# Kernel optimization log

Measured on AMD Instinct MI355X. Metric: run time of the kernel, lower is better.

The kernel has to match this reference:

```python
import jax, jax.numpy as jnp
import numpy as np

N = 65536   # total sentences
B = 8192    # number of bags (ragged scopes)
C = 1024    # class_dim
R = 100     # rel_num


def setup_inputs() -> dict:
    key = jax.random.key(0)
    k1, k2, k3, k4 = jax.random.split(key, 4)
    X = jax.random.normal(k1, (N, C), jnp.float32)            # post-fc1 sentence reps
    Constraints = jax.random.normal(k2, (R, C), jnp.float32)  # post-fc2 constraint reps
    W = jax.random.normal(k3, (R, C), jnp.float32) * 0.02     # classifier weight
    b = jnp.zeros((R,), jnp.float32)                           # classifier bias
    # ragged scopes: random cut points -> contiguous [start, end) per bag
    rng = np.random.default_rng(0)
    cuts = np.sort(rng.choice(np.arange(1, N), B - 1, replace=False))
    starts = np.concatenate([[0], cuts])
    ends = np.concatenate([cuts, [N]])
    X_Scope = jnp.asarray(np.stack([starts, ends], axis=1), jnp.int32)  # [B, 2]
    X_Rel = jax.random.randint(k4, (B,), 0, R, jnp.int32)               # [B]
    return dict(X=X, Constraints=Constraints, W=W, b=b, X_Scope=X_Scope, X_Rel=X_Rel)


def reference(X, Constraints, W, b, X_Scope, X_Rel):
    n, _ = X.shape
    nb = X_Scope.shape[0]
    # map each sentence to its (contiguous) bag via scope starts
    starts = X_Scope[:, 0]
    seg = jnp.searchsorted(starts, jnp.arange(n, dtype=starts.dtype), side='right') - 1  # [N]
    # per-sentence attention logit against its bag's relation constraint
    Con = Constraints[X_Rel]                                   # [B, C]
    scores = jnp.einsum('nc,nc->n', X, Con[seg])               # [N]
    # numerically-stable per-bag softmax
    m = jax.ops.segment_max(scores, seg, num_segments=nb)      # [B]
    e = jnp.exp(scores - m[seg])                               # [N]
    denom = jax.ops.segment_sum(e, seg, num_segments=nb)       # [B]
    w = e / denom[seg]                                         # [N]
    # attention-weighted bag pooling
    bag = jax.ops.segment_sum(w[:, None] * X, seg, num_segments=nb)  # [B, C]
    # classifier (dropout is identity at eval)
    return bag @ W.T + b                                       # [B, R]
```

## Files before the change

kernel.cpp:

```cpp
#include <hip/hip_runtime.h>
#include <math.h>

#define CDIM 1024
#define RDIM 100
#define NBAGS 8192
#define RPAD 112

typedef float floatx4 __attribute__((ext_vector_type(4)));
typedef short bf16x8 __attribute__((ext_vector_type(8)));

__device__ __forceinline__ float dot4(float4 a, float4 b) {
    return a.x * b.x + a.y * b.y + a.z * b.z + a.w * b.w;
}

__device__ __forceinline__ unsigned short f2bf(float f) {
    unsigned int u = __builtin_bit_cast(unsigned int, f);
    u += 0x7FFFu + ((u >> 16) & 1u);
    return (unsigned short)(u >> 16);
}

#define LOADROW(D0, D1, D2, D3, ri)                                          \
    {                                                                        \
        const float4* p_ = (const float4*)(X + (size_t)(ri) * CDIM);         \
        D0 = p_[lane];       D1 = p_[lane + 64];                             \
        D2 = p_[lane + 128]; D3 = p_[lane + 192];                            \
    }

#define COMPUTE_ROW(A0, A1, A2, A3)                                          \
    {                                                                        \
        float p = dot4(A0, c0) + dot4(A1, c1) + dot4(A2, c2) + dot4(A3, c3); \
        p += __shfl_xor(p, 1);                                               \
        p += __shfl_xor(p, 2);                                               \
        p += __shfl_xor(p, 4);                                               \
        p += __shfl_xor(p, 8);                                               \
        p += __shfl_xor(p, 16);                                              \
        p += __shfl_xor(p, 32);                                              \
        const float newm = fmaxf(m, p);                                      \
        const float corr = __expf(m - newm);             \
        const float wgt  = __expf(p - newm);                                 \
        denom = fmaf(denom, corr, wgt);                                      \
        a0.x = fmaf(a0.x, corr, wgt * A0.x); a0.y = fmaf(a0.y, corr, wgt * A0.y); \
        a0.z = fmaf(a0.z, corr, wgt * A0.z); a0.w = fmaf(a0.w, corr, wgt * A0.w); \
        a1.x = fmaf(a1.x, corr, wgt * A1.x); a1.y = fmaf(a1.y, corr, wgt * A1.y); \
        a1.z = fmaf(a1.z, corr, wgt * A1.z); a1.w = fmaf(a1.w, corr, wgt * A1.w); \
        a2.x = fmaf(a2.x, corr, wgt * A2.x); a2.y = fmaf(a2.y, corr, wgt * A2.y); \
        a2.z = fmaf(a2.z, corr, wgt * A2.z); a2.w = fmaf(a2.w, corr, wgt * A2.w); \
        a3.x = fmaf(a3.x, corr, wgt * A3.x); a3.y = fmaf(a3.y, corr, wgt * A3.y); \
        a3.z = fmaf(a3.z, corr, wgt * A3.z); a3.w = fmaf(a3.w, corr, wgt * A3.w); \
        m = newm;                                                            \
    }

__global__ __launch_bounds__(256) void bag_softmax_kernel(
    const float* __restrict__ X,
    const float* __restrict__ Constraints,
    const int* __restrict__ scope,
    const int* __restrict__ rel,
    const float* __restrict__ W,
    unsigned short* __restrict__ bagbuf,
    unsigned short* __restrict__ PW)
{
    const int lane = threadIdx.x & 63;
    const int w    = threadIdx.x >> 6;

    if (blockIdx.x >= NBAGS) {
        const int rr = blockIdx.x - NBAGS;
        const int t  = threadIdx.x;
        const int kc  = t >> 3;
        const int sub = (t >> 1) & 3;
        const int i0  = (t & 1) * 4;
        ushort4 o = {0, 0, 0, 0};
        if (rr < RDIM) {
            float4 v = *(const float4*)(W + (size_t)rr * CDIM + t * 4);
            o.x = f2bf(v.x); o.y = f2bf(v.y); o.z = f2bf(v.z); o.w = f2bf(v.w);
        }
        const int tt = rr >> 4, rl = rr & 15;
        *(ushort4*)(PW + ((size_t)(kc * 7 + tt) * 64 + sub * 16 + rl) * 8 + i0) = o;
        return;
    }

    __shared__ float4 lds_acc[4][256];
    __shared__ float  lds_m[4];
    __shared__ float  lds_d[4];

    const int bag = blockIdx.x;
    const int s = scope[2 * bag];
    const int e = scope[2 * bag + 1];
    const int r = rel[bag];

    const float4* conp = (const float4*)(Constraints + (size_t)r * CDIM);
    const float4 c0 = conp[lane];
    const float4 c1 = conp[lane + 64];
    const float4 c2 = conp[lane + 128];
    const float4 c3 = conp[lane + 192];

    float4 a0 = {0.f, 0.f, 0.f, 0.f};
    float4 a1 = {0.f, 0.f, 0.f, 0.f};
    float4 a2 = {0.f, 0.f, 0.f, 0.f};
    float4 a3 = {0.f, 0.f, 0.f, 0.f};
    float m = -INFINITY;
    float denom = 0.f;

    int row = s + w;
    if (row < e) {
        float4 A0, A1, A2, A3;
        float4 B0, B1, B2, B3;
        float4 C0, C1, C2, C3;

        LOADROW(A0, A1, A2, A3, row)
        if (row + 4 < e) LOADROW(B0, B1, B2, B3, row + 4)

        for (; row + 8 < e; row += 4) {
            LOADROW(C0, C1, C2, C3, row + 8)
            __builtin_amdgcn_sched_barrier(0);
            COMPUTE_ROW(A0, A1, A2, A3)
            A0 = B0; A1 = B1; A2 = B2; A3 = B3;
            B0 = C0; B1 = C1; B2 = C2; B3 = C3;
        }
        if (row + 4 < e) {
            COMPUTE_ROW(A0, A1, A2, A3)
            COMPUTE_ROW(B0, B1, B2, B3)
        } else {
            COMPUTE_ROW(A0, A1, A2, A3)
        }
    }

    if (lane == 0) { lds_m[w] = m; lds_d[w] = denom; }
    lds_acc[w][lane]       = a0;
    lds_acc[w][lane + 64]  = a1;
    lds_acc[w][lane + 128] = a2;
    lds_acc[w][lane + 192] = a3;
    __syncthreads();

    const int t = threadIdx.x;
    const float m0 = lds_m[0], m1 = lds_m[1], m2 = lds_m[2], m3 = lds_m[3];
    const float ms = fmaxf(fmaxf(m0, m1), fmaxf(m2, m3));
    const float f0 = __expf(m0 - ms);
    const float f1 = __expf(m1 - ms);
    const float f2 = __expf(m2 - ms);
    const float f3 = __expf(m3 - ms);
    const float dn = f0 * lds_d[0] + f1 * lds_d[1] + f2 * lds_d[2] + f3 * lds_d[3];
    const float inv = 1.0f / dn;

    const float4 v0 = lds_acc[0][t];
    const float4 v1 = lds_acc[1][t];
    const float4 v2 = lds_acc[2][t];
    const float4 v3 = lds_acc[3][t];
    const float ox = (f0 * v0.x + f1 * v1.x + f2 * v2.x + f3 * v3.x) * inv;
    const float oy = (f0 * v0.y + f1 * v1.y + f2 * v2.y + f3 * v3.y) * inv;
    const float oz = (f0 * v0.z + f1 * v1.z + f2 * v2.z + f3 * v3.z) * inv;
    const float ow = (f0 * v0.w + f1 * v1.w + f2 * v2.w + f3 * v3.w) * inv;

    ushort4 o;
    o.x = f2bf(ox); o.y = f2bf(oy); o.z = f2bf(oz); o.w = f2bf(ow);
    *(ushort4*)(bagbuf + (size_t)bag * CDIM + t * 4) = o;
}

__global__ __launch_bounds__(512) void bag_gemm_mfma(
    const unsigned short* __restrict__ bagbuf,
    const unsigned short* __restrict__ PW,
    const float* __restrict__ bias,
    float* __restrict__ out)
{
    const int q    = threadIdx.x >> 6;
    const int lane = threadIdx.x & 63;
    const int bag0 = blockIdx.x * 16;
    const int ln15 = lane & 15;
    const int koff = (lane >> 4) * 8;

    __shared__ floatx4 lds[8][7][64];

    floatx4 acc[7];
    #pragma unroll
    for (int t = 0; t < 7; ++t) acc[t] = (floatx4){0.f, 0.f, 0.f, 0.f};

    const unsigned short* aRow  = bagbuf + (size_t)(bag0 + ln15) * CDIM + koff;
    const unsigned short* bBase = PW + lane * 8;

    #pragma unroll
    for (int i = 0; i < 4; ++i) {
        const int kc = q * 4 + i;
        const bf16x8 a = *(const bf16x8*)(aRow + kc * 32);
        #pragma unroll
        for (int t = 0; t < 7; ++t) {
            const bf16x8 b = *(const bf16x8*)(bBase + (size_t)(kc * 7 + t) * 512);
            acc[t] = __builtin_amdgcn_mfma_f32_16x16x32_bf16(a, b, acc[t], 0, 0, 0);
        }
    }

    #pragma unroll
    for (int t = 0; t < 7; ++t) lds[q][t][lane] = acc[t];
    __syncthreads();

    const int p = threadIdx.x;
    if (p < 448) {
        const int t    = p >> 6;
        const int slot = p & 63;
        const int r    = t * 16 + (slot & 15);
        if (r < RDIM) {
            floatx4 s = lds[0][t][slot];
            #pragma unroll
            for (int qq = 1; qq < 8; ++qq) s += lds[qq][t][slot];
            const float bv = bias[r];
            const int bagr = bag0 + (slot >> 4) * 4;
            out[(size_t)(bagr + 0) * RDIM + r] = s[0] + bv;
            out[(size_t)(bagr + 1) * RDIM + r] = s[1] + bv;
            out[(size_t)(bagr + 2) * RDIM + r] = s[2] + bv;
            out[(size_t)(bagr + 3) * RDIM + r] = s[3] + bv;
        }
    }
}

extern "C" void kernel_launch(void* const* d_in, const int* in_sizes, int n_in,
                              void* d_out, int out_size, void* d_ws, size_t ws_size,
                              hipStream_t stream) {
    const float* X    = (const float*)d_in[0];
    const float* Con  = (const float*)d_in[1];
    const float* W    = (const float*)d_in[2];
    const float* bias = (const float*)d_in[3];
    const int* scope  = (const int*)d_in[4];
    const int* rel    = (const int*)d_in[5];
    float* out = (float*)d_out;

    unsigned short* bagbuf = (unsigned short*)d_ws;
    unsigned short* PW     = bagbuf + (size_t)NBAGS * CDIM;

    bag_softmax_kernel<<<NBAGS + RPAD, 256, 0, stream>>>(X, Con, scope, rel, W, bagbuf, PW);
    bag_gemm_mfma<<<NBAGS / 16, 512, 0, stream>>>(bagbuf, PW, bias, out);
}
```

Baseline: 63.86 us.

## Fuse bag softmax pooling with classifier GEMM via shared-memory bag tile

Each block now processes 16 bags in sequence. Their pooled bf16 vectors go into a swizzled shared-memory tile instead of a global workspace, and the MFMA classifier for those 16 bags runs inside the same kernel. The W conversion to packed bf16 moves to a small separate prep kernel, and the next bag's constraint row is prefetched during the current bag. This removes the global round trip for the bag buffer and the second large kernel launch. In exchange the grid drops from about 8K blocks to 512, which limits memory-level parallelism for the bandwidth-bound scan over X and serialises bags with block barriers.

```diff
diff --git a/kernel.cpp b/kernel.cpp
--- a/kernel.cpp
+++ b/kernel.cpp
@@ -5,6 +5,8 @@
 #define RDIM 100
 #define NBAGS 8192
 #define RPAD 112
+#define BPB 16
+#define NBLK (NBAGS / BPB)
 
 typedef float floatx4 __attribute__((ext_vector_type(4)));
 typedef short bf16x8 __attribute__((ext_vector_type(8)));
@@ -50,162 +52,161 @@
         m = newm;                                                            \
     }
 
-__global__ __launch_bounds__(256) void bag_softmax_kernel(
+__global__ __launch_bounds__(256) void pw_prep(
+    const float* __restrict__ W, unsigned short* __restrict__ PW)
+{
+    const int rr = blockIdx.x;
+    const int t  = threadIdx.x;
+    const int kc  = t >> 3;
+    const int sub = (t >> 1) & 3;
+    const int i0  = (t & 1) * 4;
+    ushort4 o = {0, 0, 0, 0};
+    if (rr < RDIM) {
+        float4 v = *(const float4*)(W + (size_t)rr * CDIM + t * 4);
+        o.x = f2bf(v.x); o.y = f2bf(v.y); o.z = f2bf(v.z); o.w = f2bf(v.w);
+    }
+    const int tt = rr >> 4, rl = rr & 15;
+    *(ushort4*)(PW + ((size_t)(kc * 7 + tt) * 64 + sub * 16 + rl) * 8 + i0) = o;
+}
+
+__global__ __launch_bounds__(256) void fused_kernel(
     const float* __restrict__ X,
     const float* __restrict__ Constraints,
     const int* __restrict__ scope,
     const int* __restrict__ rel,
-    const float* __restrict__ W,
-    unsigned short* __restrict__ bagbuf,
-    unsigned short* __restrict__ PW)
-{
-    const int lane = threadIdx.x & 63;
-    const int w    = threadIdx.x >> 6;
-
-    if (blockIdx.x >= NBAGS) {
-        const int rr = blockIdx.x - NBAGS;
-        const int t  = threadIdx.x;
-        const int kc  = t >> 3;
-        const int sub = (t >> 1) & 3;
-        const int i0  = (t & 1) * 4;
-        ushort4 o = {0, 0, 0, 0};
-        if (rr < RDIM) {
-            float4 v = *(const float4*)(W + (size_t)rr * CDIM + t * 4);
-            o.x = f2bf(v.x); o.y = f2bf(v.y); o.z = f2bf(v.z); o.w = f2bf(v.w);
-        }
-        const int tt = rr >> 4, rl = rr & 15;
-        *(ushort4*)(PW + ((size_t)(kc * 7 + tt) * 64 + sub * 16 + rl) * 8 + i0) = o;
-        return;
-    }
-
-    __shared__ float4 lds_acc[4][256];
-    __shared__ float  lds_m[4];
-    __shared__ float  lds_d[4];
-
-    const int bag = blockIdx.x;
-    const int s = scope[2 * bag];
-    const int e = scope[2 * bag + 1];
-    const int r = rel[bag];
-
-    const float4* conp = (const float4*)(Constraints + (size_t)r * CDIM);
-    const float4 c0 = conp[lane];
-    const float4 c1 = conp[lane + 64];
-    const float4 c2 = conp[lane + 128];
-    const float4 c3 = conp[lane + 192];
-
-    float4 a0 = {0.f, 0.f, 0.f, 0.f};
-    float4 a1 = {0.f, 0.f, 0.f, 0.f};
-    float4 a2 = {0.f, 0.f, 0.f, 0.f};
-    float4 a3 = {0.f, 0.f, 0.f, 0.f};
-    float m = -INFINITY;
-    float denom = 0.f;
-
-    int row = s + w;
-    if (row < e) {
-        float4 A0, A1, A2, A3;
-        float4 B0, B1, B2, B3;
-        float4 C0, C1, C2, C3;
-
-        LOADROW(A0, A1, A2, A3, row)
-        if (row + 4 < e) LOADROW(B0, B1, B2, B3, row + 4)
-
-        for (; row + 8 < e; row += 4) {
-            LOADROW(C0, C1, C2, C3, row + 8)
-            __builtin_amdgcn_sched_barrier(0);
-            COMPUTE_ROW(A0, A1, A2, A3)
-            A0 = B0; A1 = B1; A2 = B2; A3 = B3;
-            B0 = C0; B1 = C1; B2 = C2; B3 = C3;
-        }
-        if (row + 4 < e) {
-            COMPUTE_ROW(A0, A1, A2, A3)
-            COMPUTE_ROW(B0, B1, B2, B3)
-        } else {
-            COMPUTE_ROW(A0, A1, A2, A3)
-        }
-    }
-
-    if (lane == 0) { lds_m[w] = m; lds_d[w] = denom; }
-    lds_acc[w][lane]       = a0;
-    lds_acc[w][lane + 64]  = a1;
-    lds_acc[w][lane + 128] = a2;
-    lds_acc[w][lane + 192] = a3;
-    __syncthreads();
-
-    const int t = threadIdx.x;
-    const float m0 = lds_m[0], m1 = lds_m[1], m2 = lds_m[2], m3 = lds_m[3];
-    const float ms = fmaxf(fmaxf(m0, m1), fmaxf(m2, m3));
-    const float f0 = __expf(m0 - ms);
-    const float f1 = __expf(m1 - ms);
-    const float f2 = __expf(m2 - ms);
-    const float f3 = __expf(m3 - ms);
-    const float dn = f0 * lds_d[0] + f1 * lds_d[1] + f2 * lds_d[2] + f3 * lds_d[3];
-    const float inv = 1.0f / dn;
-
-    const float4 v0 = lds_acc[0][t];
-    const float4 v1 = lds_acc[1][t];
-    const float4 v2 = lds_acc[2][t];
-    const float4 v3 = lds_acc[3][t];
-    const float ox = (f0 * v0.x + f1 * v1.x + f2 * v2.x + f3 * v3.x) * inv;
-    const float oy = (f0 * v0.y + f1 * v1.y + f2 * v2.y + f3 * v3.y) * inv;
-    const float oz = (f0 * v0.z + f1 * v1.z + f2 * v2.z + f3 * v3.z) * inv;
-    const float ow = (f0 * v0.w + f1 * v1.w + f2 * v2.w + f3 * v3.w) * inv;
-
-    ushort4 o;
-    o.x = f2bf(ox); o.y = f2bf(oy); o.z = f2bf(oz); o.w = f2bf(ow);
-    *(ushort4*)(bagbuf + (size_t)bag * CDIM + t * 4) = o;
-}
-
-__global__ __launch_bounds__(512) void bag_gemm_mfma(
-    const unsigned short* __restrict__ bagbuf,
     const unsigned short* __restrict__ PW,
     const float* __restrict__ bias,
     float* __restrict__ out)
 {
-    const int q    = threadIdx.x >> 6;
+    __shared__ float4 mergebuf[4][256];
+    __shared__ float  lds_m[4];
+    __shared__ float  lds_d[4];
+    __shared__ unsigned short bagsm[BPB][CDIM];
+
     const int lane = threadIdx.x & 63;
-    const int bag0 = blockIdx.x * 16;
+    const int w    = threadIdx.x >> 6;
+    const int t    = threadIdx.x;
+    const int bag0 = blockIdx.x * BPB;
+
+    float4 c0, c1, c2, c3;
+    {
+        const float4* conp = (const float4*)(Constraints + (size_t)rel[bag0] * CDIM);
+        c0 = conp[lane]; c1 = conp[lane + 64]; c2 = conp[lane + 128]; c3 = conp[lane + 192];
+    }
+
+    #pragma unroll 1
+    for (int j = 0; j < BPB; ++j) {
+        const int bag = bag0 + j;
+        const int s = scope[2 * bag];
+        const int e = scope[2 * bag + 1];
+
+        float4 a0 = {0.f, 0.f, 0.f, 0.f};
+        float4 a1 = {0.f, 0.f, 0.f, 0.f};
+        float4 a2 = {0.f, 0.f, 0.f, 0.f};
+        float4 a3 = {0.f, 0.f, 0.f, 0.f};
+        float m = -INFINITY;
+        float denom = 0.f;
+
+        int row = s + w;
+        if (row < e) {
+            float4 A0, A1, A2, A3;
+            float4 B0, B1, B2, B3;
+            float4 C0, C1, C2, C3;
+
+            LOADROW(A0, A1, A2, A3, row)
+            if (row + 4 < e) LOADROW(B0, B1, B2, B3, row + 4)
+
+            for (; row + 8 < e; row += 4) {
+                LOADROW(C0, C1, C2, C3, row + 8)
+                __builtin_amdgcn_sched_barrier(0);
+                COMPUTE_ROW(A0, A1, A2, A3)
+                A0 = B0; A1 = B1; A2 = B2; A3 = B3;
+                B0 = C0; B1 = C1; B2 = C2; B3 = C3;
+            }
+            if (row + 4 < e) {
+                COMPUTE_ROW(A0, A1, A2, A3)
+                COMPUTE_ROW(B0, B1, B2, B3)
+            } else {
+                COMPUTE_ROW(A0, A1, A2, A3)
+            }
+        }
+
+        float4 n0, n1, n2, n3;
+        if (j + 1 < BPB) {
+            const float4* conp = (const float4*)(Constraints + (size_t)rel[bag + 1] * CDIM);
+            n0 = conp[lane]; n1 = conp[lane + 64]; n2 = conp[lane + 128]; n3 = conp[lane + 192];
+        }
+
+        if (lane == 0) { lds_m[w] = m; lds_d[w] = denom; }
+        mergebuf[w][lane]       = a0;
+        mergebuf[w][lane + 64]  = a1;
+        mergebuf[w][lane + 128] = a2;
+        mergebuf[w][lane + 192] = a3;
+        __syncthreads();
+
+        const float m0 = lds_m[0], m1 = lds_m[1], m2 = lds_m[2], m3 = lds_m[3];
+        const float ms = fmaxf(fmaxf(m0, m1), fmaxf(m2, m3));
+        const float f0 = __expf(m0 - ms);
+        const float f1 = __expf(m1 - ms);
+        const float f2 = __expf(m2 - ms);
+        const float f3 = __expf(m3 - ms);
+        const float dn = f0 * lds_d[0] + f1 * lds_d[1] + f2 * lds_d[2] + f3 * lds_d[3];
+        const float inv = 1.0f / dn;
+
+        const float4 v0 = mergebuf[0][t];
+        const float4 v1 = mergebuf[1][t];
+        const float4 v2 = mergebuf[2][t];
+        const float4 v3 = mergebuf[3][t];
+        const float ox = (f0 * v0.x + f1 * v1.x + f2 * v2.x + f3 * v3.x) * inv;
+        const float oy = (f0 * v0.y + f1 * v1.y + f2 * v2.y + f3 * v3.y) * inv;
+        const float oz = (f0 * v0.z + f1 * v1.z + f2 * v2.z + f3 * v3.z) * inv;
+        const float ow = (f0 * v0.w + f1 * v1.w + f2 * v2.w + f3 * v3.w) * inv;
+
+        ushort4 o;
+        o.x = f2bf(ox); o.y = f2bf(oy); o.z = f2bf(oz); o.w = f2bf(ow);
+        const int blk = (t >> 1) ^ (j & 7);
+        *(ushort4*)((char*)&bagsm[j][0] + blk * 16 + (t & 1) * 8) = o;
+        __syncthreads();
+
+        c0 = n0; c1 = n1; c2 = n2; c3 = n3;
+    }
+
     const int ln15 = lane & 15;
-    const int koff = (lane >> 4) * 8;
-
-    __shared__ floatx4 lds[8][7][64];
-
-    floatx4 acc[7];
-    #pragma unroll
-    for (int t = 0; t < 7; ++t) acc[t] = (floatx4){0.f, 0.f, 0.f, 0.f};
-
-    const unsigned short* aRow  = bagbuf + (size_t)(bag0 + ln15) * CDIM + koff;
-    const unsigned short* bBase = PW + lane * 8;
-
-    #pragma unroll
-    for (int i = 0; i < 4; ++i) {
-        const int kc = q * 4 + i;
-        const bf16x8 a = *(const bf16x8*)(aRow + kc * 32);
-        #pragma unroll
-        for (int t = 0; t < 7; ++t) {
-            const bf16x8 b = *(const bf16x8*)(bBase + (size_t)(kc * 7 + t) * 512);
-            acc[t] = __builtin_amdgcn_mfma_f32_16x16x32_bf16(a, b, acc[t], 0, 0, 0);
-        }
-    }
-
-    #pragma unroll
-    for (int t = 0; t < 7; ++t) lds[q][t][lane] = acc[t];
-    __syncthreads();
-
-    const int p = threadIdx.x;
-    if (p < 448) {
-        const int t    = p >> 6;
-        const int slot = p & 63;
-        const int r    = t * 16 + (slot & 15);
+    const int kgrp = lane >> 4;
+    const int tA = w, tB = w + 4;
+    floatx4 accA = (floatx4){0.f, 0.f, 0.f, 0.f};
+    floatx4 accB = (floatx4){0.f, 0.f, 0.f, 0.f};
+    const bool hasB = (tB < 7);
+
+    #pragma unroll 4
+    for (int kc = 0; kc < CDIM / 32; ++kc) {
+        const int swz = (kc * 4 + kgrp) ^ (ln15 & 7);
+        const bf16x8 a = *(const bf16x8*)((const char*)&bagsm[ln15][0] + swz * 16);
+        const bf16x8 bA = *(const bf16x8*)(PW + ((size_t)(kc * 7 + tA) * 64 + lane) * 8);
+        accA = __builtin_amdgcn_mfma_f32_16x16x32_bf16(a, bA, accA, 0, 0, 0);
+        if (hasB) {
+            const bf16x8 bB = *(const bf16x8*)(PW + ((size_t)(kc * 7 + tB) * 64 + lane) * 8);
+            accB = __builtin_amdgcn_mfma_f32_16x16x32_bf16(a, bB, accB, 0, 0, 0);
+        }
+    }
+
+    const int mbase = kgrp * 4;
+    {
+        const int r = tA * 16 + ln15;
         if (r < RDIM) {
-            floatx4 s = lds[0][t][slot];
+            const float bv = bias[r];
             #pragma unroll
-            for (int qq = 1; qq < 8; ++qq) s += lds[qq][t][slot];
+            for (int reg = 0; reg < 4; ++reg)
+                out[(size_t)(bag0 + mbase + reg) * RDIM + r] = accA[reg] + bv;
+        }
+    }
+    if (hasB) {
+        const int r = tB * 16 + ln15;
+        if (r < RDIM) {
             const float bv = bias[r];
-            const int bagr = bag0 + (slot >> 4) * 4;
-            out[(size_t)(bagr + 0) * RDIM + r] = s[0] + bv;
-            out[(size_t)(bagr + 1) * RDIM + r] = s[1] + bv;
-            out[(size_t)(bagr + 2) * RDIM + r] = s[2] + bv;
-            out[(size_t)(bagr + 3) * RDIM + r] = s[3] + bv;
+            #pragma unroll
+            for (int reg = 0; reg < 4; ++reg)
+                out[(size_t)(bag0 + mbase + reg) * RDIM + r] = accB[reg] + bv;
         }
     }
 }
@@ -221,9 +222,8 @@
     const int* rel    = (const int*)d_in[5];
     float* out = (float*)d_out;
 
-    unsigned short* bagbuf = (unsigned short*)d_ws;
-    unsigned short* PW     = bagbuf + (size_t)NBAGS * CDIM;
-
-    bag_softmax_kernel<<<NBAGS + RPAD, 256, 0, stream>>>(X, Con, scope, rel, W, bagbuf, PW);
-    bag_gemm_mfma<<<NBAGS / 16, 512, 0, stream>>>(bagbuf, PW, bias, out);
-}
+    unsigned short* PW = (unsigned short*)d_ws;
+
+    pw_prep<<<RPAD, 256, 0, stream>>>(W, PW);
+    fused_kernel<<<NBLK, 256, 0, stream>>>(X, Con, scope, rel, PW, bias, out);
+}
```

Measured after the change: 68.29 us. +6.9%, slower.

## Defer per-bag wave merge from softmax kernel into GEMM kernel

Applied to the files above, without the earlier changes.

Each wave of the softmax kernel now writes its unnormalized bf16 partial accumulator and its running max/denominator to global memory, instead of merging across waves through LDS with a block barrier. The GEMM kernel computes the merge scales per bag and combines the four partials on the fly while building the MFMA A operand. This removes the shared-memory staging and barrier from the bandwidth-bound pass. In exchange it adds several times more intermediate global traffic, and partials are rounded to bf16 before merging.

```diff
diff --git a/kernel.cpp b/kernel.cpp
--- a/kernel.cpp
+++ b/kernel.cpp
@@ -17,6 +17,10 @@
     unsigned int u = __builtin_bit_cast(unsigned int, f);
     u += 0x7FFFu + ((u >> 16) & 1u);
     return (unsigned short)(u >> 16);
+}
+
+__device__ __forceinline__ float bf2f(unsigned short u) {
+    return __builtin_bit_cast(float, (unsigned int)u << 16);
 }
 
 #define LOADROW(D0, D1, D2, D3, ri)                                          \
@@ -50,13 +54,14 @@
         m = newm;                                                            \
     }
 
-__global__ __launch_bounds__(256) void bag_softmax_kernel(
+__global__ __launch_bounds__(256) void bag_softmax_partial(
     const float* __restrict__ X,
     const float* __restrict__ Constraints,
     const int* __restrict__ scope,
     const int* __restrict__ rel,
     const float* __restrict__ W,
-    unsigned short* __restrict__ bagbuf,
+    unsigned short* __restrict__ partial,
+    float* __restrict__ pmd,
     unsigned short* __restrict__ PW)
 {
     const int lane = threadIdx.x & 63;
@@ -78,10 +83,6 @@
         return;
     }
 
-    __shared__ float4 lds_acc[4][256];
-    __shared__ float  lds_m[4];
-    __shared__ float  lds_d[4];
-
     const int bag = blockIdx.x;
     const int s = scope[2 * bag];
     const int e = scope[2 * bag + 1];
@@ -124,39 +125,32 @@
         }
     }
 
-    if (lane == 0) { lds_m[w] = m; lds_d[w] = denom; }
-    lds_acc[w][lane]       = a0;
-    lds_acc[w][lane + 64]  = a1;
-    lds_acc[w][lane + 128] = a2;
-    lds_acc[w][lane + 192] = a3;
-    __syncthreads();
-
-    const int t = threadIdx.x;
-    const float m0 = lds_m[0], m1 = lds_m[1], m2 = lds_m[2], m3 = lds_m[3];
-    const float ms = fmaxf(fmaxf(m0, m1), fmaxf(m2, m3));
-    const float f0 = __expf(m0 - ms);
-    const float f1 = __expf(m1 - ms);
-    const float f2 = __expf(m2 - ms);
-    const float f3 = __expf(m3 - ms);
-    const float dn = f0 * lds_d[0] + f1 * lds_d[1] + f2 * lds_d[2] + f3 * lds_d[3];
-    const float inv = 1.0f / dn;
-
-    const float4 v0 = lds_acc[0][t];
-    const float4 v1 = lds_acc[1][t];
-    const float4 v2 = lds_acc[2][t];
-    const float4 v3 = lds_acc[3][t];
-    const float ox = (f0 * v0.x + f1 * v1.x + f2 * v2.x + f3 * v3.x) * inv;
-    const float oy = (f0 * v0.y + f1 * v1.y + f2 * v2.y + f3 * v3.y) * inv;
-    const float oz = (f0 * v0.z + f1 * v1.z + f2 * v2.z + f3 * v3.z) * inv;
-    const float ow = (f0 * v0.w + f1 * v1.w + f2 * v2.w + f3 * v3.w) * inv;
-
-    ushort4 o;
-    o.x = f2bf(ox); o.y = f2bf(oy); o.z = f2bf(oz); o.w = f2bf(ow);
-    *(ushort4*)(bagbuf + (size_t)bag * CDIM + t * 4) = o;
-}
-
-__global__ __launch_bounds__(512) void bag_gemm_mfma(
-    const unsigned short* __restrict__ bagbuf,
+    if (lane == 0) {
+        pmd[bag * 8 + w * 2 + 0] = m;
+        pmd[bag * 8 + w * 2 + 1] = denom;
+    }
+    unsigned short* pr = partial + ((size_t)bag * 4 + w) * CDIM;
+    {
+        ushort4 o; o.x = f2bf(a0.x); o.y = f2bf(a0.y); o.z = f2bf(a0.z); o.w = f2bf(a0.w);
+        *(ushort4*)(pr + 4 * lane) = o;
+    }
+    {
+        ushort4 o; o.x = f2bf(a1.x); o.y = f2bf(a1.y); o.z = f2bf(a1.z); o.w = f2bf(a1.w);
+        *(ushort4*)(pr + 256 + 4 * lane) = o;
+    }
+    {
+        ushort4 o; o.x = f2bf(a2.x); o.y = f2bf(a2.y); o.z = f2bf(a2.z); o.w = f2bf(a2.w);
+        *(ushort4*)(pr + 512 + 4 * lane) = o;
+    }
+    {
+        ushort4 o; o.x = f2bf(a3.x); o.y = f2bf(a3.y); o.z = f2bf(a3.z); o.w = f2bf(a3.w);
+        *(ushort4*)(pr + 768 + 4 * lane) = o;
+    }
+}
+
+__global__ __launch_bounds__(512) void bag_gemm_merge(
+    const unsigned short* __restrict__ partial,
+    const float* __restrict__ pmd,
     const unsigned short* __restrict__ PW,
     const float* __restrict__ bias,
     float* __restrict__ out)
@@ -167,19 +161,55 @@
     const int ln15 = lane & 15;
     const int koff = (lane >> 4) * 8;
 
+    __shared__ float   smd[128];
+    __shared__ float   ssc[16][4];
     __shared__ floatx4 lds[8][7][64];
+
+    if (threadIdx.x < 128) smd[threadIdx.x] = pmd[bag0 * 8 + threadIdx.x];
+    __syncthreads();
+    if (threadIdx.x < 16) {
+        const float* pp = &smd[threadIdx.x * 8];
+        const float m0 = pp[0], d0 = pp[1], m1 = pp[2], d1 = pp[3];
+        const float m2 = pp[4], d2 = pp[5], m3 = pp[6], d3 = pp[7];
+        const float ms = fmaxf(fmaxf(m0, m1), fmaxf(m2, m3));
+        const float f0 = __expf(m0 - ms);
+        const float f1 = __expf(m1 - ms);
+        const float f2 = __expf(m2 - ms);
+        const float f3 = __expf(m3 - ms);
+        const float inv = 1.0f / (f0 * d0 + f1 * d1 + f2 * d2 + f3 * d3);
+        ssc[threadIdx.x][0] = f0 * inv;
+        ssc[threadIdx.x][1] = f1 * inv;
+        ssc[threadIdx.x][2] = f2 * inv;
+        ssc[threadIdx.x][3] = f3 * inv;
+    }
+    __syncthreads();
+
+    const float s0 = ssc[ln15][0], s1 = ssc[ln15][1];
+    const float s2 = ssc[ln15][2], s3 = ssc[ln15][3];
 
     floatx4 acc[7];
     #pragma unroll
     for (int t = 0; t < 7; ++t) acc[t] = (floatx4){0.f, 0.f, 0.f, 0.f};
 
-    const unsigned short* aRow  = bagbuf + (size_t)(bag0 + ln15) * CDIM + koff;
+    const unsigned short* aBase = partial + (size_t)(bag0 + ln15) * 4 * CDIM + koff;
     const unsigned short* bBase = PW + lane * 8;
 
     #pragma unroll
     for (int i = 0; i < 4; ++i) {
         const int kc = q * 4 + i;
-        const bf16x8 a = *(const bf16x8*)(aRow + kc * 32);
+        const bf16x8 p0 = *(const bf16x8*)(aBase + 0 * CDIM + kc * 32);
+        const bf16x8 p1 = *(const bf16x8*)(aBase + 1 * CDIM + kc * 32);
+        const bf16x8 p2 = *(const bf16x8*)(aBase + 2 * CDIM + kc * 32);
+        const bf16x8 p3 = *(const bf16x8*)(aBase + 3 * CDIM + kc * 32);
+        bf16x8 a;
+        #pragma unroll
+        for (int j = 0; j < 8; ++j) {
+            float v = s0 * bf2f((unsigned short)p0[j]);
+            v = fmaf(s1, bf2f((unsigned short)p1[j]), v);
+            v = fmaf(s2, bf2f((unsigned short)p2[j]), v);
+            v = fmaf(s3, bf2f((unsigned short)p3[j]), v);
+            a[j] = (short)f2bf(v);
+        }
         #pragma unroll
         for (int t = 0; t < 7; ++t) {
             const bf16x8 b = *(const bf16x8*)(bBase + (size_t)(kc * 7 + t) * 512);
@@ -221,9 +251,10 @@
     const int* rel    = (const int*)d_in[5];
     float* out = (float*)d_out;
 
-    unsigned short* bagbuf = (unsigned short*)d_ws;
-    unsigned short* PW     = bagbuf + (size_t)NBAGS * CDIM;
-
-    bag_softmax_kernel<<<NBAGS + RPAD, 256, 0, stream>>>(X, Con, scope, rel, W, bagbuf, PW);
-    bag_gemm_mfma<<<NBAGS / 16, 512, 0, stream>>>(bagbuf, PW, bias, out);
-}
+    unsigned short* partial = (unsigned short*)d_ws;
+    unsigned short* PW      = partial + (size_t)NBAGS * 4 * CDIM;
+    float* pmd              = (float*)(PW + (size_t)RPAD * CDIM);
+
+    bag_softmax_partial<<<NBAGS + RPAD, 256, 0, stream>>>(X, Con, scope, rel, W, partial, pmd, PW);
+    bag_gemm_merge<<<NBAGS / 16, 512, 0, stream>>>(partial, pmd, PW, bias, out);
+}
```

Measured after the change: 90.42 us. 41.6% more time.
